# Performance work log

Hardware: AMD Instinct MI355X
Metric: run time of the kernel (lower is better)

## Reference

```python
import jax, jax.numpy as jnp
import numpy as np

N_HEAD = 16
INPUT_DIM = 1024
D_K = 64


def setup_inputs() -> dict:
    key = jax.random.key(0)
    k1, k2, k3 = jax.random.split(key, 3)
    x = jax.random.normal(k1, (4, 2048, INPUT_DIM), dtype=jnp.float32)
    # xavier_uniform for linear weights
    def xavier(k, shape):
        fan_out, fan_in = shape
        limit = (6.0 / (fan_in + fan_out)) ** 0.5
        return jax.random.uniform(k, shape, jnp.float32, -limit, limit)
    W_qkv = xavier(k2, (3 * D_K * N_HEAD, INPUT_DIM))
    b_qkv = jnp.zeros((3 * D_K * N_HEAD,), jnp.float32)
    W_o = xavier(k3, (D_K * N_HEAD, D_K * N_HEAD))
    b_o = jnp.zeros((D_K * N_HEAD,), jnp.float32)
    return {"x": x, "W_qkv": W_qkv, "b_qkv": b_qkv, "W_o": W_o, "b_o": b_o}


def reference(x, W_qkv, b_qkv, W_o, b_o):
    B, S, _ = x.shape
    h = x @ W_qkv.T + b_qkv                      # (B, S, 3*d_k*H)
    # NOTE: original module reshapes directly (no transpose) to (B, H, S, 3*d_k)
    h = h.reshape(B, N_HEAD, S, 3 * D_K)
    q, k, v = jnp.split(h, 3, axis=-1)           # each (B, H, S, d_k)
    scores = jnp.einsum("bhqd,bhkd->bhqk", q, k) / jnp.sqrt(jnp.float32(D_K))
    attn = jax.nn.softmax(scores, axis=-1)       # (B, H, S, S)
    o = jnp.einsum("bhqk,bhkd->bhqd", attn, v)   # (B, H, S, d_k)
    o = o.transpose(0, 2, 1, 3).reshape(B, S, N_HEAD * D_K)
    return o @ W_o.T + b_o
```

## Files before the change

kernel.cpp:

```cpp
#include <hip/hip_runtime.h>
#include <stdint.h>


typedef __attribute__((ext_vector_type(8))) short short8;
typedef __attribute__((ext_vector_type(4))) short short4v;
typedef __attribute__((ext_vector_type(4))) float f32x4;
typedef __attribute__((ext_vector_type(16))) float f32x16;

#define B_SZ 4
#define S_SZ 2048
#define H_N 16
#define DK 64
#define IN_DIM 1024
#define QKV_DIM 3072
#define MODEL 1024
#define M_ROWS (B_SZ * S_SZ)

#define QSCALE 0.1803368801f

#if __has_builtin(__builtin_amdgcn_exp2f)
#define EXP2(x) __builtin_amdgcn_exp2f(x)
#else
#define EXP2(x) exp2f(x)
#endif

__device__ __forceinline__ short f2bf(float f) {
    union { float f; uint32_t u; } v; v.f = f;
    uint32_t r = v.u + 0x7FFFu + ((v.u >> 16) & 1u);
    return (short)(r >> 16);
}

__device__ __forceinline__ uint32_t pk2f(float a, float b) {
    union { float f; uint32_t u; } va, vb; va.f = a; vb.f = b;
    return __builtin_amdgcn_perm(vb.u + 0x8000u, va.u + 0x8000u, 0x07060302u);
}

__device__ __forceinline__ void gld_lds16(const void* g, void* l) {
    __builtin_amdgcn_global_load_lds(
        (const __attribute__((address_space(1))) void*)g,
        (__attribute__((address_space(3))) void*)l, 16, 0, 0);
}

__global__ __launch_bounds__(256) void cvt_kernel(
    const float* __restrict__ x, const float* __restrict__ wq,
    const float* __restrict__ wo, short* __restrict__ xb,
    short* __restrict__ wqb, short* __restrict__ wob) {
    const int NX = M_ROWS * IN_DIM / 4;
    const int NQ = QKV_DIM * IN_DIM / 4;
    const int NO = MODEL * IN_DIM / 4;
    const int total = NX + NQ + NO;
    for (int i = blockIdx.x * blockDim.x + threadIdx.x; i < total;
         i += gridDim.x * blockDim.x) {
        const f32x4* src; short4v* dst; int j;
        if (i < NX)           { src = (const f32x4*)x;  dst = (short4v*)xb;  j = i; }
        else if (i < NX + NQ) { src = (const f32x4*)wq; dst = (short4v*)wqb; j = i - NX; }
        else                  { src = (const f32x4*)wo; dst = (short4v*)wob; j = i - NX - NQ; }
        f32x4 v = src[j];
        short4v o;
        o[0] = f2bf(v[0]); o[1] = f2bf(v[1]); o[2] = f2bf(v[2]); o[3] = f2bf(v[3]);
        dst[j] = o;
    }
}

template <int MODE>
__global__ __launch_bounds__(256, 2) void gemm_bt(
    const short* __restrict__ A, const short* __restrict__ Bm,
    const float* __restrict__ bias, float* __restrict__ Cout,
    short* __restrict__ Qb, short* __restrict__ Kb, short* __restrict__ Vt,
    int M, int N, int K) {
    __shared__ short As[128 * 32];
    __shared__ short Bs[128 * 32];
    const int tid = threadIdx.x;
    const int wave = tid >> 6, lane = tid & 63;
    const int row16 = lane & 15, kgrp = lane >> 4;
    const int wm = (wave >> 1) * 64, wn = (wave & 1) * 64;
    const int nwg = gridDim.x * gridDim.y;
    const int id = blockIdx.y * gridDim.x + blockIdx.x;
    const int nid = (id & 7) * (nwg >> 3) + (id >> 3);
    const int bn = nid % gridDim.x, bm = nid / gridDim.x;
    const short* Ab = A + (size_t)bm * 128 * K;
    const short* Bb = Bm + (size_t)bn * 128 * K;
    f32x4 acc[4][4] = {};
    const int r0 = tid >> 2;
    const int seg = (tid & 3) * 8;
    for (int k0 = 0; k0 < K; k0 += 32) {
        gld_lds16(Ab + (size_t)r0 * K + k0 + seg, &As[r0 * 32 + seg]);
        gld_lds16(Ab + (size_t)(r0 + 64) * K + k0 + seg, &As[(r0 + 64) * 32 + seg]);
        gld_lds16(Bb + (size_t)r0 * K + k0 + seg, &Bs[r0 * 32 + seg]);
        gld_lds16(Bb + (size_t)(r0 + 64) * K + k0 + seg, &Bs[(r0 + 64) * 32 + seg]);
        __syncthreads();
        short8 af[4], bfr[4];
#pragma unroll
        for (int i = 0; i < 4; ++i)
            af[i] = *(const short8*)&As[(wm + i * 16 + row16) * 32 + kgrp * 8];
#pragma unroll
        for (int j = 0; j < 4; ++j)
            bfr[j] = *(const short8*)&Bs[(wn + j * 16 + row16) * 32 + kgrp * 8];
#pragma unroll
        for (int i = 0; i < 4; ++i)
#pragma unroll
            for (int j = 0; j < 4; ++j)
                acc[i][j] = __builtin_amdgcn_mfma_f32_16x16x32_bf16(
                    af[i], bfr[j], acc[i][j], 0, 0, 0);
        __syncthreads();
    }
#pragma unroll
    for (int j = 0; j < 4; ++j) {
        int gcol = bn * 128 + wn + j * 16 + row16;
        float bv = bias[gcol];
#pragma unroll
        for (int i = 0; i < 4; ++i) {
#pragma unroll
            for (int r = 0; r < 4; ++r) {
                int grow = bm * 128 + wm + i * 16 + kgrp * 4 + r;
                float val = acc[i][j][r] + bv;
                if (MODE == 1) {
                    Cout[(size_t)grow * N + gcol] = val;
                } else {
                    int b = grow >> 11, so = grow & 2047;
                    int hh = so >> 7, a = so & 127;
                    int rr = gcol / 192, cc = gcol - rr * 192;
                    int ss = a * 16 + rr;
                    int bh = b * H_N + hh;
                    if (cc < 64) {
                        Qb[(((size_t)bh) * S_SZ + ss) * DK + cc] = f2bf(val * QSCALE);
                    } else if (cc < 128) {
                        Kb[(((size_t)bh) * S_SZ + ss) * DK + cc - 64] = f2bf(val);
                    } else {
                        Vt[((size_t)bh * DK + (cc - 128)) * S_SZ + ss] = f2bf(val);
                    }
                }
            }
        }
    }
}

__global__ __launch_bounds__(256, 4) void attn_kernel(
    const short* __restrict__ Qg, const short* __restrict__ Kg,
    const short* __restrict__ Vtg, short* __restrict__ O) {
    __shared__ short Ks[2][64 * 64];
    __shared__ short Vs[2][64 * 64];
    const int tid = threadIdx.x;
    const int wave = tid >> 6, lane = tid & 63;
    const int q = lane & 31, hi = lane >> 5;
    const int id = blockIdx.x;
    const int bh = (id & 7) * 8 + ((id >> 3) & 7);
    const int qt = id >> 6;
    const int b = bh >> 4, h = bh & 15;
    const short* Qp = Qg + (size_t)bh * S_SZ * DK;
    const short* Kp = Kg + (size_t)bh * S_SZ * DK;
    const short* Vp = Vtg + (size_t)bh * DK * S_SZ;
    const int q0 = qt * 128 + wave * 32;

    short8 qf[4];
#pragma unroll
    for (int c = 0; c < 4; ++c)
        qf[c] = *(const short8*)&Qp[(size_t)(q0 + q) * DK + c * 16 + hi * 8];

    f32x16 ot0 = {}, ot1 = {};
    float m_run = -1e30f, l_run = 0.f;

    const int srow0 = wave * 16 + (lane >> 3);
    const int srow1 = srow0 + 8;
    const int sc0 = ((lane & 7) ^ (srow0 & 7)) * 8;
    const int sc1 = ((lane & 7) ^ (srow1 & 7)) * 8;
#define STAGE(BUF, KV0)                                                         \
    {                                                                           \
        gld_lds16(Kp + (size_t)((KV0) + srow0) * DK + sc0,                      \
                  &Ks[BUF][(wave * 16) * 64]);                                  \
        gld_lds16(Kp + (size_t)((KV0) + srow1) * DK + sc1,                      \
                  &Ks[BUF][(wave * 16 + 8) * 64]);                              \
        gld_lds16(Vp + (size_t)srow0 * S_SZ + (KV0) + sc0,                      \
                  &Vs[BUF][(wave * 16) * 64]);                                  \
        gld_lds16(Vp + (size_t)srow1 * S_SZ + (KV0) + sc1,                      \
                  &Vs[BUF][(wave * 16 + 8) * 64]);                              \
    }

    STAGE(0, 0);

    const int NT = S_SZ / 64;
    for (int t = 0; t < NT; ++t) {
        __syncthreads();
        const int cur = t & 1;
        if (t + 1 < NT) STAGE(cur ^ 1, (t + 1) * 64);

        const int qx = (q & 7) << 3;
        f32x16 st0 = {}, st1 = {};
        __builtin_amdgcn_s_setprio(1);
#pragma unroll
        for (int c = 0; c < 4; ++c) {
            const int sw = (((c * 2 + hi) << 3) ^ qx);
            short8 kf0 = *(const short8*)&Ks[cur][q * 64 + sw];
            short8 kf1 = *(const short8*)&Ks[cur][(32 + q) * 64 + sw];
            st0 = __builtin_amdgcn_mfma_f32_32x32x16_bf16(kf0, qf[c], st0, 0, 0, 0);
            st1 = __builtin_amdgcn_mfma_f32_32x32x16_bf16(kf1, qf[c], st1, 0, 0, 0);
        }
        __builtin_amdgcn_s_setprio(0);

        float ma = fmaxf(st0[0], st1[0]), mb = fmaxf(st0[1], st1[1]);
        float mc = fmaxf(st0[2], st1[2]), md = fmaxf(st0[3], st1[3]);
#pragma unroll
        for (int r = 4; r < 16; r += 4) {
            ma = fmaxf(ma, fmaxf(st0[r], st1[r]));
            mb = fmaxf(mb, fmaxf(st0[r + 1], st1[r + 1]));
            mc = fmaxf(mc, fmaxf(st0[r + 2], st1[r + 2]));
            md = fmaxf(md, fmaxf(st0[r + 3], st1[r + 3]));
        }
        float pm = fmaxf(fmaxf(ma, mb), fmaxf(mc, md));
        pm = fmaxf(pm, __shfl_xor(pm, 32));
        if (__any(pm > m_run + 8.f)) {
            float mnew = fmaxf(m_run, pm);
            float corr = EXP2(m_run - mnew);
            m_run = mnew;
            l_run *= corr;
#pragma unroll
            for (int r = 0; r < 16; ++r) { ot0[r] *= corr; ot1[r] *= corr; }
        }
        float s0 = 0.f, s1 = 0.f, s2 = 0.f, s3 = 0.f;
#pragma unroll
        for (int r = 0; r < 16; r += 4) {
            st0[r] = EXP2(st0[r] - m_run);         s0 += st0[r];
            st0[r + 1] = EXP2(st0[r + 1] - m_run); s1 += st0[r + 1];
            st0[r + 2] = EXP2(st0[r + 2] - m_run); s2 += st0[r + 2];
            st0[r + 3] = EXP2(st0[r + 3] - m_run); s3 += st0[r + 3];
        }
#pragma unroll
        for (int r = 0; r < 16; r += 4) {
            st1[r] = EXP2(st1[r] - m_run);         s0 += st1[r];
            st1[r + 1] = EXP2(st1[r + 1] - m_run); s1 += st1[r + 1];
            st1[r + 2] = EXP2(st1[r + 2] - m_run); s2 += st1[r + 2];
            st1[r + 3] = EXP2(st1[r + 3] - m_run); s3 += st1[r + 3];
        }
        float ssum = (s0 + s1) + (s2 + s3);
        ssum += __shfl_xor(ssum, 32);
        l_run += ssum;

        __builtin_amdgcn_s_setprio(1);
#if __has_builtin(__builtin_amdgcn_permlane32_swap)
#define PVCHUNK(ST, B0, CH)                                                    \
    {                                                                          \
        uint32_t A01 = pk2f(ST[(B0) + 0], ST[(B0) + 1]);                       \
        uint32_t A23 = pk2f(ST[(B0) + 2], ST[(B0) + 3]);                       \
        uint32_t B45 = pk2f(ST[(B0) + 4], ST[(B0) + 5]);                       \
        uint32_t B67 = pk2f(ST[(B0) + 6], ST[(B0) + 7]);                       \
        auto sw0 = __builtin_amdgcn_permlane32_swap(A01, B45, false, false);   \
        auto sw1 = __builtin_amdgcn_permlane32_swap(A23, B67, false, false);   \
        union { uint32_t u[4]; short8 s8; } pbu;                               \
        pbu.u[0] = sw0[0]; pbu.u[1] = sw1[0];                                  \
        pbu.u[2] = sw0[1]; pbu.u[3] = sw1[1];                                  \
        const int vsw = ((((CH) * 2 + hi) << 3) ^ qx);                         \
        short8 vf0 = *(const short8*)&Vs[cur][q * 64 + vsw];                   \
        short8 vf1 = *(const short8*)&Vs[cur][(32 + q) * 64 + vsw];            \
        ot0 = __builtin_amdgcn_mfma_f32_32x32x16_bf16(vf0, pbu.s8, ot0, 0, 0, 0); \
        ot1 = __builtin_amdgcn_mfma_f32_32x32x16_bf16(vf1, pbu.s8, ot1, 0, 0, 0); \
    }
#else
#define PVCHUNK(ST, B0, CH)                                                    \
    {                                                                          \
        uint32_t A01 = pk2f(ST[(B0) + 0], ST[(B0) + 1]);                       \
        uint32_t A23 = pk2f(ST[(B0) + 2], ST[(B0) + 3]);                       \
        uint32_t B45 = pk2f(ST[(B0) + 4], ST[(B0) + 5]);                       \
        uint32_t B67 = pk2f(ST[(B0) + 6], ST[(B0) + 7]);                       \
        uint32_t t0 = hi ? A01 : B45, t1 = hi ? A23 : B67;                     \
        uint32_t r0 = (uint32_t)__shfl_xor((int)t0, 32);                       \
        uint32_t r1 = (uint32_t)__shfl_xor((int)t1, 32);                       \
        union { uint32_t u[4]; short8 s8; } pbu;                               \
        pbu.u[0] = hi ? r0 : A01; pbu.u[1] = hi ? r1 : A23;                    \
        pbu.u[2] = hi ? B45 : r0; pbu.u[3] = hi ? B67 : r1;                    \
        const int vsw = ((((CH) * 2 + hi) << 3) ^ qx);                         \
        short8 vf0 = *(const short8*)&Vs[cur][q * 64 + vsw];                   \
        short8 vf1 = *(const short8*)&Vs[cur][(32 + q) * 64 + vsw];            \
        ot0 = __builtin_amdgcn_mfma_f32_32x32x16_bf16(vf0, pbu.s8, ot0, 0, 0, 0); \
        ot1 = __builtin_amdgcn_mfma_f32_32x32x16_bf16(vf1, pbu.s8, ot1, 0, 0, 0); \
    }
#endif
        PVCHUNK(st0, 0, 0);
        PVCHUNK(st0, 8, 1);
        PVCHUNK(st1, 0, 2);
        PVCHUNK(st1, 8, 3);
#undef PVCHUNK
        __builtin_amdgcn_s_setprio(0);
    }
#undef STAGE

    float inv = 1.f / l_run;
    size_t rowbase = ((size_t)b * S_SZ + (q0 + q)) * MODEL + h * DK;
#pragma unroll
    for (int i = 0; i < 4; ++i) {
        short4v v0, v1;
#pragma unroll
        for (int jj = 0; jj < 4; ++jj) {
            v0[jj] = f2bf(ot0[4 * i + jj] * inv);
            v1[jj] = f2bf(ot1[4 * i + jj] * inv);
        }
        *(short4v*)&O[rowbase + 8 * i + 4 * hi] = v0;
        *(short4v*)&O[rowbase + 32 + 8 * i + 4 * hi] = v1;
    }
}

extern "C" void kernel_launch(void* const* d_in, const int* in_sizes, int n_in,
                              void* d_out, int out_size, void* d_ws, size_t ws_size,
                              hipStream_t stream) {
    const float* x    = (const float*)d_in[0];
    const float* Wqkv = (const float*)d_in[1];
    const float* bqkv = (const float*)d_in[2];
    const float* Wo   = (const float*)d_in[3];
    const float* bo   = (const float*)d_in[4];
    float* out = (float*)d_out;
    char* ws = (char*)d_ws;

    short* xb  = (short*)(ws + 0);
    short* wqb = (short*)(ws + 16777216);
    short* wob = (short*)(ws + 23068672);
    short* Qb  = (short*)(ws + 25165824);
    short* Kb  = (short*)(ws + 41943040);
    short* Vt  = (short*)(ws + 58720256);
    short* Ob  = (short*)(ws + 0);

    cvt_kernel<<<dim3(2048), dim3(256), 0, stream>>>(x, Wqkv, Wo, xb, wqb, wob);
    gemm_bt<0><<<dim3(QKV_DIM / 128, M_ROWS / 128), dim3(256), 0, stream>>>(
        xb, wqb, bqkv, nullptr, Qb, Kb, Vt, M_ROWS, QKV_DIM, IN_DIM);
    attn_kernel<<<dim3(1024), dim3(256), 0, stream>>>(Qb, Kb, Vt, Ob);
    gemm_bt<1><<<dim3(MODEL / 128, M_ROWS / 128), dim3(256), 0, stream>>>(
        Ob, wob, bo, out, nullptr, nullptr, nullptr, M_ROWS, MODEL, IN_DIM);
}
```

Measured before the change: 239.2 us.

## Double-buffer GEMM LDS tiles with BK=64, XOR swizzle, and prefetch

The bf16 GEMM now uses two LDS buffers with a K-tile of 64 instead of 32. It prefetches the next tile via global-to-LDS loads while computing on the current one, which removes one barrier per iteration and overlaps memory with MFMA. An XOR swizzle on the 16-byte chunks reduces LDS bank conflicts on fragment reads, and s_setprio raises wave priority around the MFMA block. LDS use grows to 64KB per block, which may limit the two-blocks-per-CU occupancy target.

```diff
diff --git a/kernel.cpp b/kernel.cpp
--- a/kernel.cpp
+++ b/kernel.cpp
@@ -68,8 +68,8 @@
     const float* __restrict__ bias, float* __restrict__ Cout,
     short* __restrict__ Qb, short* __restrict__ Kb, short* __restrict__ Vt,
     int M, int N, int K) {
-    __shared__ short As[128 * 32];
-    __shared__ short Bs[128 * 32];
+    __shared__ short As[2][128 * 64];
+    __shared__ short Bs[2][128 * 64];
     const int tid = threadIdx.x;
     const int wave = tid >> 6, lane = tid & 63;
     const int row16 = lane & 15, kgrp = lane >> 4;
@@ -81,29 +81,51 @@
     const short* Ab = A + (size_t)bm * 128 * K;
     const short* Bb = Bm + (size_t)bn * 128 * K;
     f32x4 acc[4][4] = {};
-    const int r0 = tid >> 2;
-    const int seg = (tid & 3) * 8;
-    for (int k0 = 0; k0 < K; k0 += 32) {
-        gld_lds16(Ab + (size_t)r0 * K + k0 + seg, &As[r0 * 32 + seg]);
-        gld_lds16(Ab + (size_t)(r0 + 64) * K + k0 + seg, &As[(r0 + 64) * 32 + seg]);
-        gld_lds16(Bb + (size_t)r0 * K + k0 + seg, &Bs[r0 * 32 + seg]);
-        gld_lds16(Bb + (size_t)(r0 + 64) * K + k0 + seg, &Bs[(r0 + 64) * 32 + seg]);
+
+    const int soff = ((lane & 7) ^ (lane >> 3)) * 8;
+#define GSTAGE(BUF, K0)                                                        \
+    {                                                                          \
+        _Pragma("unroll") for (int l = 0; l < 4; ++l) {                        \
+            int r = wave * 8 + (lane >> 3) + l * 32;                           \
+            gld_lds16(Ab + (size_t)r * K + (K0) + soff,                        \
+                      &As[BUF][(wave * 8 + l * 32) * 64]);                     \
+            gld_lds16(Bb + (size_t)r * K + (K0) + soff,                        \
+                      &Bs[BUF][(wave * 8 + l * 32) * 64]);                     \
+        }                                                                      \
+    }
+
+    GSTAGE(0, 0);
+    const int NK = K >> 6;
+    for (int t = 0; t < NK; ++t) {
         __syncthreads();
-        short8 af[4], bfr[4];
-#pragma unroll
-        for (int i = 0; i < 4; ++i)
-            af[i] = *(const short8*)&As[(wm + i * 16 + row16) * 32 + kgrp * 8];
-#pragma unroll
-        for (int j = 0; j < 4; ++j)
-            bfr[j] = *(const short8*)&Bs[(wn + j * 16 + row16) * 32 + kgrp * 8];
-#pragma unroll
-        for (int i = 0; i < 4; ++i)
-#pragma unroll
-            for (int j = 0; j < 4; ++j)
-                acc[i][j] = __builtin_amdgcn_mfma_f32_16x16x32_bf16(
-                    af[i], bfr[j], acc[i][j], 0, 0, 0);
-        __syncthreads();
-    }
+        const int cur = t & 1;
+        if (t + 1 < NK) GSTAGE(cur ^ 1, (t + 1) * 64);
+#pragma unroll
+        for (int kk = 0; kk < 2; ++kk) {
+            short8 af[4], bfr[4];
+#pragma unroll
+            for (int i = 0; i < 4; ++i) {
+                int R = wm + i * 16 + row16;
+                int ch = (kk * 4 + kgrp) ^ (R & 7);
+                af[i] = *(const short8*)&As[cur][R * 64 + ch * 8];
+            }
+#pragma unroll
+            for (int j = 0; j < 4; ++j) {
+                int R = wn + j * 16 + row16;
+                int ch = (kk * 4 + kgrp) ^ (R & 7);
+                bfr[j] = *(const short8*)&Bs[cur][R * 64 + ch * 8];
+            }
+            __builtin_amdgcn_s_setprio(1);
+#pragma unroll
+            for (int i = 0; i < 4; ++i)
+#pragma unroll
+                for (int j = 0; j < 4; ++j)
+                    acc[i][j] = __builtin_amdgcn_mfma_f32_16x16x32_bf16(
+                        af[i], bfr[j], acc[i][j], 0, 0, 0);
+            __builtin_amdgcn_s_setprio(0);
+        }
+    }
+#undef GSTAGE
 #pragma unroll
     for (int j = 0; j < 4; ++j) {
         int gcol = bn * 128 + wn + j * 16 + row16;
```

New measurement: 232.7 us. 1.03x faster.
